# Performance work log

Hardware: AMD Instinct MI355X
Metric: run time of the kernel (lower is better)

The kernel has to match this reference:

```python
import jax, jax.numpy as jnp
import numpy as np
import math

D_MODEL = 1024
N_HEAD = 16
D_HEAD = D_MODEL // N_HEAD
B, T = 2, 2048


def setup_inputs() -> dict:
    key = jax.random.key(0)
    k1, k2, k3, k4, k5 = jax.random.split(key, 5)
    x = jax.random.normal(k1, (B, T, D_MODEL), dtype=jnp.float32)
    # causal mask: 1 where attending allowed (lower triangular), broadcastable [1,1,T,T]
    mask = jnp.tril(jnp.ones((T, T), dtype=jnp.int32))[None, None, :, :]
    scale = 1.0 / math.sqrt(D_MODEL)
    qkv_w = jax.random.normal(k2, (D_MODEL, 3 * D_MODEL), dtype=jnp.float32) * scale
    qkv_b = jnp.zeros((3 * D_MODEL,), dtype=jnp.float32)
    proj_w = jax.random.normal(k3, (D_MODEL, D_MODEL), dtype=jnp.float32) * scale
    proj_b = jnp.zeros((D_MODEL,), dtype=jnp.float32)
    return {"x": x, "mask": mask, "qkv_w": qkv_w, "qkv_b": qkv_b,
            "proj_w": proj_w, "proj_b": proj_b}


def reference(x, mask, qkv_w, qkv_b, proj_w, proj_b):
    Bs, Ts, C = x.shape
    qkv = x @ qkv_w + qkv_b                      # [B,T,3C]
    q, k, v = jnp.split(qkv, 3, axis=-1)
    # [B,T,C] -> [B,H,T,Dh]
    def heads(t):
        return t.reshape(Bs, Ts, N_HEAD, D_HEAD).transpose(0, 2, 1, 3)
    q, k, v = heads(q), heads(k), heads(v)
    scores = jnp.einsum('bhtd,bhsd->bhts', q, k) / math.sqrt(D_HEAD)
    scores = jnp.where(mask == 0, jnp.float32(-1e9), scores)
    attn = jax.nn.softmax(scores, axis=-1)
    out = jnp.einsum('bhts,bhsd->bhtd', attn, v)  # [B,H,T,Dh]
    out = out.transpose(0, 2, 1, 3).reshape(Bs, Ts, C)
    return out @ proj_w + proj_b
```

## Files before the change

### kernel.cpp

```cpp
#include <hip/hip_runtime.h>
#include <hip/hip_bf16.h>
#include <stdint.h>

typedef float f32x4 __attribute__((ext_vector_type(4)));
typedef float f32x16 __attribute__((ext_vector_type(16)));
typedef __bf16 bf16x8 __attribute__((ext_vector_type(8)));
typedef unsigned int uint2v __attribute__((ext_vector_type(2)));

#define D_MODEL 1024
#define NHEAD 16
#define DHEAD 64
#define BATCH 2
#define SEQ 2048
#define MROWS (BATCH*SEQ)
#define N3 (3*D_MODEL)

#define SCALE_LOG2E 0.1803368801111244f

__device__ __forceinline__ unsigned short f2bf(float f) {
  unsigned int u = __float_as_uint(f);
  u += 0x7FFF + ((u >> 16) & 1);
  return (unsigned short)(u >> 16);
}

#define CVTPK(d, x, y) asm("v_cvt_pk_bf16_f32 %0, %1, %2" : "=v"(d) : "v"(x), "v"(y))
#define SWAP32(x, y) do { uint2v _r = __builtin_amdgcn_permlane32_swap((x), (y), false, false); \
                          (x) = _r[0]; (y) = _r[1]; } while (0)

__device__ __forceinline__ void gload_lds16(const void* g, void* l) {
  __builtin_amdgcn_global_load_lds(
      (const __attribute__((address_space(1))) unsigned int*)g,
      (__attribute__((address_space(3))) unsigned int*)l, 16, 0, 0);
}

__global__ __launch_bounds__(256) void cvt_f32_bf16(const float* __restrict__ in,
                                                    unsigned short* __restrict__ out, int n4) {
  int i = blockIdx.x*blockDim.x + threadIdx.x;
  int stride = gridDim.x*blockDim.x;
  for (; i < n4; i += stride) {
    float4 f = ((const float4*)in)[i];
    ushort4 u;
    u.x = f2bf(f.x); u.y = f2bf(f.y); u.z = f2bf(f.z); u.w = f2bf(f.w);
    ((ushort4*)out)[i] = u;
  }
}

__global__ __launch_bounds__(256) void transpose_cvt2(const float* __restrict__ qkvw,
                                                      unsigned short* __restrict__ oq,
                                                      const float* __restrict__ projw,
                                                      unsigned short* __restrict__ op) {
  __shared__ float tile[32][33];
  int id = blockIdx.x;
  const float* in; unsigned short* out; int K, N, n0, k0;
  if (id < 3072) { in = qkvw;  out = oq; K = 1024; N = 3072; n0 = (id % 96)*32; k0 = (id / 96)*32; }
  else { id -= 3072; in = projw; out = op; K = 1024; N = 1024; n0 = (id % 32)*32; k0 = (id / 32)*32; }
  int tx = threadIdx.x & 31, ty = threadIdx.x >> 5;
#pragma unroll
  for (int i = 0; i < 4; ++i)
    tile[ty + 8*i][tx] = in[(size_t)(k0 + ty + 8*i)*N + n0 + tx];
  __syncthreads();
#pragma unroll
  for (int i = 0; i < 4; ++i)
    out[(size_t)(n0 + ty + 8*i)*K + k0 + tx] = f2bf(tile[tx][ty + 8*i]);
}

#define BM 128
#define BN 128
#define BK 64

__global__ __launch_bounds__(256, 3) void gemm_bt(
    const unsigned short* __restrict__ A,
    const unsigned short* __restrict__ Bt,
    const float* __restrict__ bias,
    int K, int N, int mode,
    unsigned short* __restrict__ qo,
    unsigned short* __restrict__ ko,
    unsigned short* __restrict__ vo,
    float* __restrict__ fo)
{
  __shared__ unsigned short a_lds[BM*BK];
  __shared__ unsigned short b_lds[BN*BK];
  int tid = threadIdx.x;
  int lane = tid & 63, wid = tid >> 6;
  int wr = wid >> 1, wc = wid & 1;
  int lr = lane & 15, lh = lane >> 4;

  int bid = blockIdx.y*gridDim.x + blockIdx.x;
  int cN = gridDim.x >> 3;
  int xcd = bid & 7;
  int j = (bid >> 3) % cN;
  int m = bid / (cN << 3);
  int M0 = m*BM, N0 = (xcd*cN + j)*BN;

  int srow = tid >> 3;
  int scol = (((tid & 7) ^ ((tid >> 3) & 7)))*8;
  const unsigned short* aP = A  + (size_t)(M0 + srow)*K + scol;
  const unsigned short* bP = Bt + (size_t)(N0 + srow)*K + scol;
  char* aL = (char*)a_lds + wid*1024;
  char* bL = (char*)b_lds + wid*1024;

  int KT = K/BK;

  f32x4 acc[4][4];
#pragma unroll
  for (int i = 0; i < 4; ++i)
#pragma unroll
    for (int j2 = 0; j2 < 4; ++j2) acc[i][j2] = (f32x4){0.f, 0.f, 0.f, 0.f};

  for (int kt = 0; kt < KT; ++kt) {
    const unsigned short* ap = aP + kt*BK;
    const unsigned short* bp = bP + kt*BK;
#pragma unroll
    for (int i = 0; i < 4; ++i) {
      gload_lds16(ap + (size_t)32*i*K, aL + i*4096);
      gload_lds16(bp + (size_t)32*i*K, bL + i*4096);
    }
    __syncthreads();
#pragma unroll
    for (int ks = 0; ks < 2; ++ks) {
      bf16x8 af[4], bf[4];
#pragma unroll
      for (int mi = 0; mi < 4; ++mi)
        af[mi] = *(const bf16x8*)&a_lds[(wr*64 + mi*16 + lr)*BK + (((ks*4 + lh) ^ (lr & 7))*8)];
#pragma unroll
      for (int ni = 0; ni < 4; ++ni)
        bf[ni] = *(const bf16x8*)&b_lds[(wc*64 + ni*16 + lr)*BK + (((ks*4 + lh) ^ (lr & 7))*8)];
#pragma unroll
      for (int mi = 0; mi < 4; ++mi)
#pragma unroll
        for (int ni = 0; ni < 4; ++ni)
          acc[mi][ni] = __builtin_amdgcn_mfma_f32_16x16x32_bf16(af[mi], bf[ni], acc[mi][ni], 0, 0, 0);
    }
    __syncthreads();
  }

#pragma unroll
  for (int mi = 0; mi < 4; ++mi) {
#pragma unroll
    for (int ni = 0; ni < 4; ++ni) {
      int ncol = N0 + wc*64 + ni*16 + lr;
      float bs = bias[ncol];
      int mbase = M0 + wr*64 + mi*16 + lh*4;
      if (mode == 0) {
        if (ncol < D_MODEL) {
          int h = ncol >> 6, d = ncol & 63;
#pragma unroll
          for (int r = 0; r < 4; ++r) {
            int mrow = mbase + r;
            int b = mrow >> 11, t = mrow & (SEQ-1);
            qo[(((size_t)(b*NHEAD + h))*SEQ + t)*DHEAD + d] =
                f2bf((acc[mi][ni][r] + bs) * SCALE_LOG2E);
          }
        } else if (ncol < 2*D_MODEL) {
          int c = ncol - D_MODEL, h = c >> 6, d = c & 63;
#pragma unroll
          for (int r = 0; r < 4; ++r) {
            int mrow = mbase + r;
            int b = mrow >> 11, t = mrow & (SEQ-1);
            ko[(((size_t)(b*NHEAD + h))*SEQ + t)*DHEAD + d] = f2bf(acc[mi][ni][r] + bs);
          }
        } else {
          int c = ncol - 2*D_MODEL, h = c >> 6, d = c & 63;
          int b = mbase >> 11, t = mbase & (SEQ-1);
          ushort4 u;
          u.x = f2bf(acc[mi][ni][0] + bs);
          u.y = f2bf(acc[mi][ni][1] + bs);
          u.z = f2bf(acc[mi][ni][2] + bs);
          u.w = f2bf(acc[mi][ni][3] + bs);
          *(ushort4*)&vo[(((size_t)(b*NHEAD + h))*DHEAD + d)*SEQ + t] = u;
        }
      } else {
#pragma unroll
        for (int r = 0; r < 4; ++r) {
          int mrow = mbase + r;
          fo[(size_t)mrow*N + ncol] = acc[mi][ni][r] + bs;
        }
      }
    }
  }
}

#define NQT128 (SEQ/128)

__global__ __launch_bounds__(256, 3) void attn_fwd(
    const unsigned short* __restrict__ q,
    const unsigned short* __restrict__ kk,
    const unsigned short* __restrict__ vt,
    unsigned short* __restrict__ out)
{
  __shared__ __align__(16) char smem[2][16384];

  int tid = threadIdx.x, lane = tid & 63, wid = tid >> 6;
  int idx = blockIdx.x;
  int qt = (NQT128 - 1) - (idx >> 5);
  int bh = idx & 31;
  int b = bh >> 4, h = bh & 15;
  int q0w = qt*128 + wid*32;
  int l31 = lane & 31, hl = lane >> 5;

  const unsigned short* qb = q  + ((size_t)bh*SEQ)*DHEAD;
  const unsigned short* kb = kk + ((size_t)bh*SEQ)*DHEAD;
  const unsigned short* vb = vt + ((size_t)bh*DHEAD)*SEQ;

  int srow = lane >> 3;
  int sslot = (lane & 7) ^ srow;

  int roff[2][4];
#pragma unroll
  for (int j = 0; j < 2; ++j)
#pragma unroll
    for (int st = 0; st < 4; ++st)
      roff[j][st] = (j*32 + l31)*128 + (((2*st + hl) ^ (l31 & 7))*16);

  bf16x8 qf[4];
#pragma unroll
  for (int st = 0; st < 4; ++st)
    qf[st] = *(const bf16x8*)(qb + (size_t)(q0w + l31)*DHEAD + st*16 + hl*8);

  f32x16 o0, o1;
#pragma unroll
  for (int i = 0; i < 16; ++i) { o0[i] = 0.f; o1[i] = 0.f; }
  float l = 0.f;
  int qg = q0w + l31;

  int nkv = 2*qt + 2;

#define STAGE(bufi, kvbase) do {                                                   \
    char* kd = smem[bufi] + wid*2048;                                              \
    char* vd = smem[bufi] + 8192 + wid*2048;                                       \
    _Pragma("unroll")                                                              \
    for (int i = 0; i < 2; ++i) {                                                  \
      gload_lds16(kb + (size_t)((kvbase) + wid*16 + i*8 + srow)*DHEAD + sslot*8,   \
                  kd + i*1024);                                                    \
      gload_lds16(vb + (size_t)(wid*16 + i*8 + srow)*SEQ + (kvbase) + sslot*8,     \
                  vd + i*1024);                                                    \
    }                                                                              \
  } while (0)

  STAGE(0, 0);
  __syncthreads();

  for (int t = 0; t < nkv; ++t) {
    int cur = t & 1;
    if (t + 1 < nkv) STAGE(cur ^ 1, (t+1)*64);
    int kv0 = t*64;

    if (kv0 <= q0w + 31) {
      const char* kbase = smem[cur];
      const char* vbase = smem[cur] + 8192;

      f32x16 s0, s1;
#pragma unroll
      for (int i = 0; i < 16; ++i) { s0[i] = 0.f; s1[i] = 0.f; }

#pragma unroll
      for (int st = 0; st < 4; ++st) {
        bf16x8 k0 = *(const bf16x8*)(kbase + roff[0][st]);
        bf16x8 k1 = *(const bf16x8*)(kbase + roff[1][st]);
        s0 = __builtin_amdgcn_mfma_f32_32x32x16_bf16(k0, qf[st], s0, 0, 0, 0);
        s1 = __builtin_amdgcn_mfma_f32_32x32x16_bf16(k1, qf[st], s1, 0, 0, 0);
      }

      if (kv0 + 63 > qg - 31) {
#pragma unroll
        for (int r = 0; r < 16; ++r) {
          int kl = (r&3) + 8*(r>>2) + 4*hl;
          if (kv0 + kl      > qg) s0[r] = -1e30f;
          if (kv0 + 32 + kl > qg) s1[r] = -1e30f;
        }
      }

#pragma unroll
      for (int j = 0; j < 2; ++j) {
        const f32x16& sj = j ? s1 : s0;
        float p[16];
#pragma unroll
        for (int r = 0; r < 16; ++r) p[r] = __builtin_amdgcn_exp2f(sj[r]);
        float t0 = (p[0]+p[1]) + (p[2]+p[3]);
        float t1 = (p[4]+p[5]) + (p[6]+p[7]);
        float t2 = (p[8]+p[9]) + (p[10]+p[11]);
        float t3 = (p[12]+p[13]) + (p[14]+p[15]);
        l += (t0+t1) + (t2+t3);
        uint32_t a0,a1,a2,a3,b0,b1,b2,b3;
        CVTPK(a0, p[0],  p[1]);  CVTPK(a1, p[2],  p[3]);
        CVTPK(b0, p[4],  p[5]);  CVTPK(b1, p[6],  p[7]);
        CVTPK(a2, p[8],  p[9]);  CVTPK(a3, p[10], p[11]);
        CVTPK(b2, p[12], p[13]); CVTPK(b3, p[14], p[15]);
        SWAP32(a0, b0); SWAP32(a1, b1); SWAP32(a2, b2); SWAP32(a3, b3);
        union { uint32_t u[4]; bf16x8 v; } pf0, pf1;
        pf0.u[0]=a0; pf0.u[1]=a1; pf0.u[2]=b0; pf0.u[3]=b1;
        pf1.u[0]=a2; pf1.u[1]=a3; pf1.u[2]=b2; pf1.u[3]=b3;
        bf16x8 v00 = *(const bf16x8*)(vbase + roff[0][2*j]);
        bf16x8 v01 = *(const bf16x8*)(vbase + roff[1][2*j]);
        bf16x8 v10 = *(const bf16x8*)(vbase + roff[0][2*j + 1]);
        bf16x8 v11 = *(const bf16x8*)(vbase + roff[1][2*j + 1]);
        o0 = __builtin_amdgcn_mfma_f32_32x32x16_bf16(v00, pf0.v, o0, 0, 0, 0);
        o1 = __builtin_amdgcn_mfma_f32_32x32x16_bf16(v01, pf0.v, o1, 0, 0, 0);
        o0 = __builtin_amdgcn_mfma_f32_32x32x16_bf16(v10, pf1.v, o0, 0, 0, 0);
        o1 = __builtin_amdgcn_mfma_f32_32x32x16_bf16(v11, pf1.v, o1, 0, 0, 0);
      }
    }
    __syncthreads();
  }
#undef STAGE

  l += __shfl_xor(l, 32);
  float inv = 1.f / l;
  o0 *= inv; o1 *= inv;

  size_t rowoff = ((size_t)(b*SEQ) + q0w + l31)*D_MODEL + h*DHEAD + hl*4;
#pragma unroll
  for (int g = 0; g < 4; ++g) {
    uint32_t w0, w1;
    CVTPK(w0, o0[4*g],   o0[4*g+1]);
    CVTPK(w1, o0[4*g+2], o0[4*g+3]);
    uint2 pk0 = {w0, w1};
    *(uint2*)(out + rowoff + 8*g) = pk0;
    CVTPK(w0, o1[4*g],   o1[4*g+1]);
    CVTPK(w1, o1[4*g+2], o1[4*g+3]);
    uint2 pk1 = {w0, w1};
    *(uint2*)(out + rowoff + 32 + 8*g) = pk1;
  }
}

extern "C" void kernel_launch(void* const* d_in, const int* in_sizes, int n_in,
                              void* d_out, int out_size, void* d_ws, size_t ws_size,
                              hipStream_t stream) {
  const float* x      = (const float*)d_in[0];
  const float* qkv_w  = (const float*)d_in[2];
  const float* qkv_b  = (const float*)d_in[3];
  const float* proj_w = (const float*)d_in[4];
  const float* proj_b = (const float*)d_in[5];

  const size_t MB = 1024*1024;
  if (ws_size < 48*MB) return;
  char* w = (char*)d_ws;
  unsigned short* xb      = (unsigned short*)(w);
  unsigned short* wqkv_t  = (unsigned short*)(w + 8*MB);
  unsigned short* wproj_t = (unsigned short*)(w + 14*MB);
  unsigned short* qbuf    = (unsigned short*)(w + 16*MB);
  unsigned short* kbuf    = (unsigned short*)(w + 24*MB);
  unsigned short* vtbuf   = (unsigned short*)(w + 32*MB);
  unsigned short* aout    = (unsigned short*)(w + 40*MB);

  cvt_f32_bf16<<<2048, 256, 0, stream>>>(x, xb, MROWS*D_MODEL/4);
  transpose_cvt2<<<4096, 256, 0, stream>>>(qkv_w, wqkv_t, proj_w, wproj_t);
  gemm_bt<<<dim3(N3/BN, MROWS/BM), 256, 0, stream>>>(xb, wqkv_t, qkv_b, D_MODEL, N3, 0,
                                                     qbuf, kbuf, vtbuf, nullptr);
  attn_fwd<<<dim3(32*NQT128), 256, 0, stream>>>(qbuf, kbuf, vtbuf, aout);
  gemm_bt<<<dim3(D_MODEL/BN, MROWS/BM), 256, 0, stream>>>(aout, wproj_t, proj_b, D_MODEL, D_MODEL, 1,
                                                          nullptr, nullptr, nullptr, (float*)d_out);
}
```

Measured before the change: 106.4 us.

## Stage QKV and attention epilogues through LDS for coalesced 16-byte stores; merge prep kernels

The QKV GEMM epilogue now writes bf16 results into swizzled shared memory first, then emits 16-byte coalesced stores to the Q/K head-major buffers and the transposed V buffer. Before, these were scattered 2-byte or 8-byte writes. The attention kernel likewise stages its output tile in LDS before writing full 128-byte rows. The two preprocessing kernels are merged into one launch. This adds an extra LDS round trip and a barrier per block in exchange for far fewer, wider global write transactions and one fewer launch.

```diff
diff --git a/kernel.cpp b/kernel.cpp
--- a/kernel.cpp
+++ b/kernel.cpp
@@ -33,24 +33,27 @@
       (__attribute__((address_space(3))) unsigned int*)l, 16, 0, 0);
 }
 
-__global__ __launch_bounds__(256) void cvt_f32_bf16(const float* __restrict__ in,
-                                                    unsigned short* __restrict__ out, int n4) {
-  int i = blockIdx.x*blockDim.x + threadIdx.x;
-  int stride = gridDim.x*blockDim.x;
-  for (; i < n4; i += stride) {
-    float4 f = ((const float4*)in)[i];
-    ushort4 u;
-    u.x = f2bf(f.x); u.y = f2bf(f.y); u.z = f2bf(f.z); u.w = f2bf(f.w);
-    ((ushort4*)out)[i] = u;
-  }
-}
-
-__global__ __launch_bounds__(256) void transpose_cvt2(const float* __restrict__ qkvw,
-                                                      unsigned short* __restrict__ oq,
-                                                      const float* __restrict__ projw,
-                                                      unsigned short* __restrict__ op) {
+__global__ __launch_bounds__(256) void prep(const float* __restrict__ x,
+                                            unsigned short* __restrict__ xb,
+                                            const float* __restrict__ qkvw,
+                                            unsigned short* __restrict__ oq,
+                                            const float* __restrict__ projw,
+                                            unsigned short* __restrict__ op) {
+  int bid = blockIdx.x;
+  if (bid < 2048) {
+    int n4 = MROWS*D_MODEL/4;
+    int i = bid*256 + threadIdx.x;
+    int stride = 2048*256;
+    for (; i < n4; i += stride) {
+      float4 f = ((const float4*)x)[i];
+      ushort4 u;
+      u.x = f2bf(f.x); u.y = f2bf(f.y); u.z = f2bf(f.z); u.w = f2bf(f.w);
+      ((ushort4*)xb)[i] = u;
+    }
+    return;
+  }
   __shared__ float tile[32][33];
-  int id = blockIdx.x;
+  int id = bid - 2048;
   const float* in; unsigned short* out; int K, N, n0, k0;
   if (id < 3072) { in = qkvw;  out = oq; K = 1024; N = 3072; n0 = (id % 96)*32; k0 = (id / 96)*32; }
   else { id -= 3072; in = projw; out = op; K = 1024; N = 1024; n0 = (id % 32)*32; k0 = (id / 32)*32; }
@@ -78,8 +81,9 @@
     unsigned short* __restrict__ vo,
     float* __restrict__ fo)
 {
-  __shared__ unsigned short a_lds[BM*BK];
-  __shared__ unsigned short b_lds[BN*BK];
+  __shared__ unsigned short lds_all[BM*BK + BN*BK];
+  unsigned short* a_lds = lds_all;
+  unsigned short* b_lds = lds_all + BM*BK;
   int tid = threadIdx.x;
   int lane = tid & 63, wid = tid >> 6;
   int wr = wid >> 1, wc = wid & 1;
@@ -134,48 +138,64 @@
     __syncthreads();
   }
 
+  if (mode == 1) {
+#pragma unroll
+    for (int mi = 0; mi < 4; ++mi) {
+#pragma unroll
+      for (int ni = 0; ni < 4; ++ni) {
+        int ncol = N0 + wc*64 + ni*16 + lr;
+        float bs = bias[ncol];
+        int mbase = M0 + wr*64 + mi*16 + lh*4;
+#pragma unroll
+        for (int r = 0; r < 4; ++r)
+          fo[(size_t)(mbase + r)*N + ncol] = acc[mi][ni][r] + bs;
+      }
+    }
+    return;
+  }
+
+  int region = N0 >> 10;
+  unsigned short* c = lds_all;
 #pragma unroll
   for (int mi = 0; mi < 4; ++mi) {
 #pragma unroll
     for (int ni = 0; ni < 4; ++ni) {
-      int ncol = N0 + wc*64 + ni*16 + lr;
-      float bs = bias[ncol];
-      int mbase = M0 + wr*64 + mi*16 + lh*4;
-      if (mode == 0) {
-        if (ncol < D_MODEL) {
-          int h = ncol >> 6, d = ncol & 63;
-#pragma unroll
-          for (int r = 0; r < 4; ++r) {
-            int mrow = mbase + r;
-            int b = mrow >> 11, t = mrow & (SEQ-1);
-            qo[(((size_t)(b*NHEAD + h))*SEQ + t)*DHEAD + d] =
-                f2bf((acc[mi][ni][r] + bs) * SCALE_LOG2E);
-          }
-        } else if (ncol < 2*D_MODEL) {
-          int c = ncol - D_MODEL, h = c >> 6, d = c & 63;
-#pragma unroll
-          for (int r = 0; r < 4; ++r) {
-            int mrow = mbase + r;
-            int b = mrow >> 11, t = mrow & (SEQ-1);
-            ko[(((size_t)(b*NHEAD + h))*SEQ + t)*DHEAD + d] = f2bf(acc[mi][ni][r] + bs);
-          }
-        } else {
-          int c = ncol - 2*D_MODEL, h = c >> 6, d = c & 63;
-          int b = mbase >> 11, t = mbase & (SEQ-1);
-          ushort4 u;
-          u.x = f2bf(acc[mi][ni][0] + bs);
-          u.y = f2bf(acc[mi][ni][1] + bs);
-          u.z = f2bf(acc[mi][ni][2] + bs);
-          u.w = f2bf(acc[mi][ni][3] + bs);
-          *(ushort4*)&vo[(((size_t)(b*NHEAD + h))*DHEAD + d)*SEQ + t] = u;
-        }
-      } else {
-#pragma unroll
-        for (int r = 0; r < 4; ++r) {
-          int mrow = mbase + r;
-          fo[(size_t)mrow*N + ncol] = acc[mi][ni][r] + bs;
-        }
-      }
+      int n = wc*64 + ni*16 + lr;
+      float bs = bias[N0 + n];
+#pragma unroll
+      for (int r = 0; r < 4; ++r) {
+        int mm = wr*64 + mi*16 + lh*4 + r;
+        float v = acc[mi][ni][r] + bs;
+        if (region == 0) v *= SCALE_LOG2E;
+        unsigned short u = f2bf(v);
+        if (region < 2)
+          c[mm*128 + ((((n >> 3) ^ (mm & 7)) << 3) | (n & 7))] = u;
+        else
+          c[n*128 + ((((mm >> 3) ^ (n & 7)) << 3) | (mm & 7))] = u;
+      }
+    }
+  }
+  __syncthreads();
+
+#pragma unroll
+  for (int it = 0; it < 8; ++it) {
+    int idx = it*256 + tid;
+    int s = idx & 7;
+    int chunk = idx >> 3;
+    int row = chunk >> 1, half = chunk & 1;
+    int4 v4 = *(const int4*)&c[row*128 + (((half*8 + s) ^ (row & 7)) << 3)];
+    if (region < 2) {
+      int tg = M0 + row;
+      int b = tg >> 11, tt = tg & (SEQ-1);
+      int h = (((N0 & 1023)) + half*64) >> 6;
+      unsigned short* dst = (region == 0) ? qo : ko;
+      *(int4*)(dst + (((size_t)(b*NHEAD + h))*SEQ + tt)*DHEAD + s*8) = v4;
+    } else {
+      int cgl = (N0 - 2*D_MODEL) + row;
+      int h = cgl >> 6, d = cgl & 63;
+      int tg = M0 + half*64 + s*8;
+      int b = tg >> 11, tt = tg & (SEQ-1);
+      *(int4*)(vo + (((size_t)(b*NHEAD + h))*DHEAD + d)*SEQ + tt) = v4;
     }
   }
 }
@@ -308,18 +328,30 @@
   float inv = 1.f / l;
   o0 *= inv; o1 *= inv;
 
-  size_t rowoff = ((size_t)(b*SEQ) + q0w + l31)*D_MODEL + h*DHEAD + hl*4;
+  unsigned short* obuf = (unsigned short*)smem;
+  int qrow = wid*32 + l31;
+  int xk = (qrow & 7) << 1;
 #pragma unroll
   for (int g = 0; g < 4; ++g) {
     uint32_t w0, w1;
     CVTPK(w0, o0[4*g],   o0[4*g+1]);
     CVTPK(w1, o0[4*g+2], o0[4*g+3]);
     uint2 pk0 = {w0, w1};
-    *(uint2*)(out + rowoff + 8*g) = pk0;
+    *(uint2*)&obuf[qrow*64 + (((2*g + hl) ^ xk) << 2)] = pk0;
     CVTPK(w0, o1[4*g],   o1[4*g+1]);
     CVTPK(w1, o1[4*g+2], o1[4*g+3]);
     uint2 pk1 = {w0, w1};
-    *(uint2*)(out + rowoff + 32 + 8*g) = pk1;
+    *(uint2*)&obuf[qrow*64 + (((8 + 2*g + hl) ^ xk) << 2)] = pk1;
+  }
+  __syncthreads();
+
+#pragma unroll
+  for (int it = 0; it < 4; ++it) {
+    int idx2 = it*256 + tid;
+    int s = idx2 & 7, row = idx2 >> 3;
+    int4 v4 = *(const int4*)&obuf[row*64 + ((s ^ (row & 7)) << 3)];
+    int tq = qt*128 + row;
+    *(int4*)(out + ((size_t)(b*SEQ) + tq)*D_MODEL + h*DHEAD + s*8) = v4;
   }
 }
 
@@ -343,8 +375,7 @@
   unsigned short* vtbuf   = (unsigned short*)(w + 32*MB);
   unsigned short* aout    = (unsigned short*)(w + 40*MB);
 
-  cvt_f32_bf16<<<2048, 256, 0, stream>>>(x, xb, MROWS*D_MODEL/4);
-  transpose_cvt2<<<4096, 256, 0, stream>>>(qkv_w, wqkv_t, proj_w, wproj_t);
+  prep<<<6144, 256, 0, stream>>>(x, xb, qkv_w, wqkv_t, proj_w, wproj_t);
   gemm_bt<<<dim3(N3/BN, MROWS/BM), 256, 0, stream>>>(xb, wqkv_t, qkv_b, D_MODEL, N3, 0,
                                                      qbuf, kbuf, vtbuf, nullptr);
   attn_fwd<<<dim3(32*NQT128), 256, 0, stream>>>(qbuf, kbuf, vtbuf, aout);
```

New measurement: 102.2 us. 1.04x faster.
